# Performance work log

Measured on AMD Instinct MI355X. Metric: run time of the kernel, lower is better.

Reference implementation:

```python
import jax, jax.numpy as jnp
import numpy as np

B, S, E, H, MAXLEN = 2, 2048, 1024, 16, 2048


def _level_indices(seq_len: int, base: int = 2) -> np.ndarray:
    """Vectorized version of get_level_index_weak over the full (target, source) grid.
    indices[t, s] = min(level, 2) for s < t, else 0. Runs in O(log S) passes."""
    tt = np.broadcast_to(np.arange(seq_len)[:, None], (seq_len, seq_len)).astype(np.int64).copy()
    ss = np.broadcast_to(np.arange(seq_len)[None, :], (seq_len, seq_len)).astype(np.int64).copy()
    res = np.zeros((seq_len, seq_len), np.int64)
    done = ~(ss < tt)  # only source < target positions get a level; rest stay 0
    while not done.all():
        l = np.floor(np.log2(np.maximum(tt, 1).astype(np.float64))).astype(np.int64)
        v = (np.int64(1) << l)
        hit = (~done) & (ss < v)
        res[hit] = l[hit] + 1
        done |= hit
        step = ~done
        tt[step] -= v[step]
        ss[step] -= v[step]
    return np.minimum(res, 2).astype(np.int32)


def setup_inputs() -> dict:
    key = jax.random.key(0)
    ks = jax.random.split(key, 10)
    sc = 0.02
    return {
        "x": jax.random.normal(ks[0], (B, S, E), dtype=jnp.float32),
        "attention_mask": jax.random.randint(ks[1], (B, S), 0, 2, dtype=jnp.int32),
        "level_indices": jnp.asarray(_level_indices(S, 2)),
        "Wq": jax.random.normal(ks[2], (E, E), dtype=jnp.float32) * sc,
        "bq": jnp.zeros((E,), jnp.float32),
        "Wk": jax.random.normal(ks[3], (E, E), dtype=jnp.float32) * sc,
        "bk": jnp.zeros((E,), jnp.float32),
        "Wv": jax.random.normal(ks[4], (E, E), dtype=jnp.float32) * sc,
        "bv": jnp.zeros((E,), jnp.float32),
        "hier": jax.random.normal(ks[5], (MAXLEN, H, 3), dtype=jnp.float32),
        "Wo": jax.random.normal(ks[6], (E, E), dtype=jnp.float32) * sc,
        "bo": jnp.zeros((E,), jnp.float32),
    }


def reference(x, attention_mask, level_indices, Wq, bq, Wk, bk, Wv, bv, hier, Wo, bo):
    b, s, e = x.shape
    h = hier.shape[1]
    dh = e // h
    # q/k are computed by the original module but never used; kept for fidelity (zero grads).
    q = x @ Wq.T + bq
    k = x @ Wk.T + bk
    v = (x @ Wv.T + bv).reshape(b, s, h, dh).transpose(0, 2, 1, 3)  # [B,H,S,Dh]
    lev = level_indices[:s, :s]  # [S,S] int, values in {0,1,2}
    # Faithful torch.gather semantics: weights[b,h,i,j] = hier[b, h, lev[i,j]]
    w3 = hier[:b]                      # [B,H,3]
    weights = w3[:, :, lev]            # [B,H,S,S]
    decay = jnp.power(jnp.float32(0.5), lev.astype(x.dtype))  # [S,S]
    weights = weights * decay
    weights = weights / (jnp.sum(weights, axis=-1, keepdims=True) + 1e-8)
    weights = jnp.where(attention_mask[:, None, None, :] == 0, jnp.float32(0.0), weights)
    out = jnp.einsum('bhij,bhjd->bhid', weights, v)  # [B,H,S,Dh]
    out = out.transpose(0, 2, 1, 3).reshape(b, s, e)
    return out @ Wo.T + bo
```

## Files before the change

### kernel.cpp

```cpp
#include <hip/hip_runtime.h>
#include <cstdint>
#include <cstddef>

constexpr int Sn = 2048;
constexpr int En = 1024;
constexpr int Bn = 2;
constexpr int Hn = 16;
constexpr int CHUNK = 32;
constexpr int NCH = Sn / CHUNK;
constexpr int Mtot = Bn * Sn;
constexpr int GCH = Mtot / CHUNK;

typedef __bf16 bf16x8 __attribute__((ext_vector_type(8)));
typedef float  f32x4  __attribute__((ext_vector_type(4)));

__device__ __forceinline__ unsigned short f2bf(float f) {
    union { float f; uint32_t u; } v; v.f = f;
    const uint32_t u = v.u;
    return (unsigned short)((u + 0x7fffu + ((u >> 16) & 1u)) >> 16);
}
__device__ __forceinline__ float bf2f(unsigned short s) {
    union { uint32_t u; float f; } v; v.u = (uint32_t)s << 16; return v.f;
}

constexpr int XN = Bn * Sn * En;
constexpr int WN = En * En;

__global__ __launch_bounds__(256)
void cast2(const float* __restrict__ x, const float* __restrict__ Wv,
           unsigned short* __restrict__ xb, unsigned short* __restrict__ Wvb)
{
    const int i = (blockIdx.x * 256 + threadIdx.x) * 4;
    const float* src; unsigned short* dst; int off;
    if (i < XN) { src = x;  dst = xb;  off = i; }
    else        { src = Wv; dst = Wvb; off = i - XN; }
    const float4 v = *(const float4*)(src + off);
    ushort4 o;
    o.x = f2bf(v.x); o.y = f2bf(v.y); o.z = f2bf(v.z); o.w = f2bf(v.w);
    *(ushort4*)(dst + off) = o;
}

#define LOAD6(k0, r0, r1, r2, r3, r4, r5)            \
    r0 = *(const uint4*)(gA0 + (k0));                \
    r1 = *(const uint4*)(gA0 + (k0) + 32);           \
    r2 = *(const uint4*)(gA1 + (k0));                \
    r3 = *(const uint4*)(gA1 + (k0) + 32);           \
    r4 = *(const uint4*)(gB0 + (k0));                \
    r5 = *(const uint4*)(gB0 + (k0) + 32);

#define STORE6B(B, r0, r1, r2, r3, r4, r5)                       \
    *(uint4*)&As[B][(rg0 * 2 + 0) * 512 + lane * 8] = r0;        \
    *(uint4*)&As[B][(rg0 * 2 + 1) * 512 + lane * 8] = r1;        \
    *(uint4*)&As[B][(rg1 * 2 + 0) * 512 + lane * 8] = r2;        \
    *(uint4*)&As[B][(rg1 * 2 + 1) * 512 + lane * 8] = r3;        \
    *(uint4*)&Bs[B][(wv  * 2 + 0) * 512 + lane * 8] = r4;        \
    *(uint4*)&Bs[B][(wv  * 2 + 1) * 512 + lane * 8] = r5;

#define COMPUTEB(B)                                                                            \
    {                                                                                          \
        bf16x8 af[4][2], bfr[2][2];                                                            \
        _Pragma("unroll")                                                                      \
        for (int i = 0; i < 4; ++i)                                                            \
            _Pragma("unroll")                                                                  \
            for (int kh = 0; kh < 2; ++kh)                                                     \
                af[i][kh] = *(const bf16x8*)&As[B][((wr * 4 + i) * 2 + kh) * 512 + lane * 8];   \
        _Pragma("unroll")                                                                      \
        for (int j = 0; j < 2; ++j)                                                            \
            _Pragma("unroll")                                                                  \
            for (int kh = 0; kh < 2; ++kh)                                                     \
                bfr[j][kh] = *(const bf16x8*)&Bs[B][((wc * 2 + j) * 2 + kh) * 512 + lane * 8]; \
        _Pragma("unroll")                                                                      \
        for (int kh = 0; kh < 2; ++kh)                                                         \
            _Pragma("unroll")                                                                  \
            for (int i = 0; i < 4; ++i)                                                        \
                _Pragma("unroll")                                                              \
                for (int j = 0; j < 2; ++j)                                                    \
                    acc[i][j] = __builtin_amdgcn_mfma_f32_16x16x32_bf16(af[i][kh], bfr[j][kh], \
                                                                        acc[i][j], 0, 0, 0);   \
    }

template<bool APPLY_MASK, bool OUT_BF16, bool FUSE_CSUM>
__global__ __launch_bounds__(256)
void gemm_pipe(const unsigned short* __restrict__ A, const unsigned short* __restrict__ Bw,
               const float* __restrict__ bias, const int* __restrict__ mask,
               void* __restrict__ Cv, float* __restrict__ csum)
{
    __shared__ __align__(16) unsigned short As[2][128 * 64];
    __shared__ __align__(16) unsigned short Bs[2][64 * 64];

    const int tid  = threadIdx.x;
    const int lane = tid & 63;
    const int wv   = tid >> 6;
    const int wr   = wv >> 1;
    const int wc   = wv & 1;
    const int id   = blockIdx.y * 16 + blockIdx.x;
    const int xcd  = id & 7;
    const int slot = id >> 3;
    const int by   = xcd * 4 + (slot >> 4);
    const int bx   = slot & 15;
    const int bm   = by * 128;
    const int bn   = bx * 64;
    const int m16  = lane & 15;
    const int kq   = lane >> 4;

    f32x4 acc[4][2] = {};

    const int rg0 = 2 * wv, rg1 = 2 * wv + 1;
    const unsigned short* gA0 = A  + (size_t)(bm + 16 * rg0 + m16) * En + kq * 8;
    const unsigned short* gA1 = A  + (size_t)(bm + 16 * rg1 + m16) * En + kq * 8;
    const unsigned short* gB0 = Bw + (size_t)(bn + 16 * wv  + m16) * En + kq * 8;

    uint4 p0, p1, p2, p3, p4, p5;
    uint4 q0, q1, q2, q3, q4, q5;

    LOAD6(0,  p0, p1, p2, p3, p4, p5);
    STORE6B(0, p0, p1, p2, p3, p4, p5);
    LOAD6(64, q0, q1, q2, q3, q4, q5);
    __syncthreads();

#pragma unroll 1
    for (int it = 0; it < 7; ++it) {
        const int kb = it * 128;
        LOAD6(kb + 128, p0, p1, p2, p3, p4, p5);
        COMPUTEB(0);
        STORE6B(1, q0, q1, q2, q3, q4, q5);
        __syncthreads();
        LOAD6(kb + 192, q0, q1, q2, q3, q4, q5);
        COMPUTEB(1);
        STORE6B(0, p0, p1, p2, p3, p4, p5);
        __syncthreads();
    }
    COMPUTEB(0);
    STORE6B(1, q0, q1, q2, q3, q4, q5);
    __syncthreads();
    COMPUTEB(1);

    float colsum[2][2] = {{0.0f, 0.0f}, {0.0f, 0.0f}};
#pragma unroll
    for (int i = 0; i < 4; ++i) {
        const int r0_ = bm + wr * 64 + i * 16 + kq * 4;
#pragma unroll
        for (int j = 0; j < 2; ++j) {
            const int c0 = bn + wc * 32 + j * 16 + m16;
            const float bcol = bias[c0];
#pragma unroll
            for (int r = 0; r < 4; ++r) {
                const int row = r0_ + r;
                float val = acc[i][j][r] + bcol;
                if (APPLY_MASK) val = (mask[row] == 0) ? 0.0f : val;
                if (FUSE_CSUM) colsum[i >> 1][j] += val;
                if (OUT_BF16)
                    ((unsigned short*)Cv)[(size_t)row * En + c0] = f2bf(val);
                else
                    ((float*)Cv)[(size_t)row * En + c0] = val;
            }
        }
    }

    if (FUSE_CSUM) {
        const int gc0 = 4 * by + 2 * wr;
#pragma unroll
        for (int g = 0; g < 2; ++g)
#pragma unroll
            for (int j = 0; j < 2; ++j) {
                float s = colsum[g][j];
                s += __shfl_xor(s, 16, 64);
                s += __shfl_xor(s, 32, 64);
                if (kq == 0)
                    csum[(size_t)(gc0 + g) * En + bn + wc * 32 + j * 16 + m16] = s;
            }
    }
}

__global__ __launch_bounds__(256)
void combine(const unsigned short* __restrict__ vm, const float* __restrict__ csum,
             const float* __restrict__ hier, const float* __restrict__ Wo,
             unsigned short* __restrict__ Wob, unsigned short* __restrict__ opre)
{
    __shared__ __align__(16) unsigned short tile[CHUNK * 256];

    const int tid = threadIdx.x;
    const int ec0 = blockIdx.x * 256;
    const int c   = blockIdx.y;
    const int b   = blockIdx.z;

    {
        const int lane16 = tid & 31;
        const int rbase  = tid >> 5;
        const size_t g0 = ((size_t)b * Sn + c * CHUNK) * En + ec0 + lane16 * 8;
#pragma unroll
        for (int r4 = 0; r4 < 4; ++r4) {
            const int row = r4 * 8 + rbase;
            *(uint4*)&tile[row * 256 + lane16 * 8] =
                *(const uint4*)(vm + g0 + (size_t)row * En);
        }
    }

    {
        const int fid = (blockIdx.z * 64 + blockIdx.y) * 4 + blockIdx.x;
        const int base = fid * 2048 + tid * 4;
#pragma unroll
        for (int half = 0; half < 2; ++half) {
            const int off = base + half * 1024;
            const float4 v = *(const float4*)(Wo + off);
            ushort4 o;
            o.x = f2bf(v.x); o.y = f2bf(v.y); o.z = f2bf(v.z); o.w = f2bf(v.w);
            *(ushort4*)(Wob + off) = o;
        }
    }

    const int e = ec0 + tid;
    const int h = e >> 6;
    const float w0 = hier[((size_t)b * Hn + h) * 3 + 0];
    const float w1 = hier[((size_t)b * Hn + h) * 3 + 1] * 0.5f;
    const float w2 = hier[((size_t)b * Hn + h) * 3 + 2] * 0.25f;

    float run = 0.0f, T = 0.0f;
    {
        const float* cp = csum + (size_t)b * NCH * En + e;
#pragma unroll 16
        for (int c2 = 0; c2 < NCH; ++c2) {
            const float v = cp[(size_t)c2 * En];
            T += v;
            run += (c2 < c) ? v : 0.0f;
        }
    }

    __syncthreads();

    float prev = 0.0f;
    const size_t base = ((size_t)b * Sn + c * CHUNK) * En + e;

#pragma unroll
    for (int t = 0; t < CHUNK; ++t) {
        const int i = c * CHUNK + t;
        const float cur = bf2f(tile[t * 256 + tid]);
        float num, Z;
        if (i & 1) {
            num = w2 * (run - prev) + w1 * prev + w0 * (T - run);
            Z = (float)(i - 1) * w2 + w1 + (float)(Sn - i) * w0 + 1e-8f;
        } else {
            num = w2 * run + w0 * (T - run);
            Z = (float)i * w2 + (float)(Sn - i) * w0 + 1e-8f;
        }
        opre[base + (size_t)t * En] = f2bf(num / Z);
        run += cur;
        prev = cur;
    }
}

extern "C" void kernel_launch(void* const* d_in, const int* in_sizes, int n_in,
                              void* d_out, int out_size, void* d_ws, size_t ws_size,
                              hipStream_t stream)
{
    const float* x    = (const float*)d_in[0];
    const int*   mask = (const int*)d_in[1];
    const float* Wv   = (const float*)d_in[7];
    const float* bv   = (const float*)d_in[8];
    const float* hier = (const float*)d_in[9];
    const float* Wo   = (const float*)d_in[10];
    const float* bo   = (const float*)d_in[11];
    float* out = (float*)d_out;

    char* ws = (char*)d_ws;
    unsigned short* xb    = (unsigned short*)ws;  ws += (size_t)Mtot * En * 2;
    unsigned short* Wvb   = (unsigned short*)ws;  ws += (size_t)En * En * 2;
    unsigned short* Wob   = (unsigned short*)ws;  ws += (size_t)En * En * 2;
    unsigned short* vmb   = (unsigned short*)ws;  ws += (size_t)Mtot * En * 2;
    float*          csum  = (float*)ws;           ws += (size_t)GCH * En * 4;
    unsigned short* opreb = (unsigned short*)ws;  ws += (size_t)Mtot * En * 2;

    dim3 threads(256);

    cast2<<<dim3((XN + WN) / 1024), threads, 0, stream>>>(x, Wv, xb, Wvb);

    dim3 gemm_grid(16, 32);

    gemm_pipe<true, true, true><<<gemm_grid, threads, 0, stream>>>(xb, Wvb, bv, mask, vmb, csum);
    combine<<<dim3(En / 256, NCH, Bn), threads, 0, stream>>>(vmb, csum, hier, Wo, Wob, opreb);
    gemm_pipe<false, false, false><<<gemm_grid, threads, 0, stream>>>(opreb, Wob, bo, nullptr, out, nullptr);
}
```

Baseline: 163.1 us.

## Replace LDS double-buffered GEMM with direct global-to-register fragment loads

Removes the shared-memory staging and double-buffer pipeline in both GEMMs; each wave now loads its MFMA operand fragments directly from global memory. This removes LDS stores, LDS reads and block barriers, and frees LDS for occupancy. In exchange, A and B tiles are no longer shared across waves in a block, which raises global/L2 traffic and exposes load latency with less explicit prefetching.

New measurement: 211.1 us. 1.29x slower.

```diff
diff --git a/kernel.cpp b/kernel.cpp
--- a/kernel.cpp
+++ b/kernel.cpp
@@ -40,54 +40,12 @@
     *(ushort4*)(dst + off) = o;
 }
 
-#define LOAD6(k0, r0, r1, r2, r3, r4, r5)            \
-    r0 = *(const uint4*)(gA0 + (k0));                \
-    r1 = *(const uint4*)(gA0 + (k0) + 32);           \
-    r2 = *(const uint4*)(gA1 + (k0));                \
-    r3 = *(const uint4*)(gA1 + (k0) + 32);           \
-    r4 = *(const uint4*)(gB0 + (k0));                \
-    r5 = *(const uint4*)(gB0 + (k0) + 32);
-
-#define STORE6B(B, r0, r1, r2, r3, r4, r5)                       \
-    *(uint4*)&As[B][(rg0 * 2 + 0) * 512 + lane * 8] = r0;        \
-    *(uint4*)&As[B][(rg0 * 2 + 1) * 512 + lane * 8] = r1;        \
-    *(uint4*)&As[B][(rg1 * 2 + 0) * 512 + lane * 8] = r2;        \
-    *(uint4*)&As[B][(rg1 * 2 + 1) * 512 + lane * 8] = r3;        \
-    *(uint4*)&Bs[B][(wv  * 2 + 0) * 512 + lane * 8] = r4;        \
-    *(uint4*)&Bs[B][(wv  * 2 + 1) * 512 + lane * 8] = r5;
-
-#define COMPUTEB(B)                                                                            \
-    {                                                                                          \
-        bf16x8 af[4][2], bfr[2][2];                                                            \
-        _Pragma("unroll")                                                                      \
-        for (int i = 0; i < 4; ++i)                                                            \
-            _Pragma("unroll")                                                                  \
-            for (int kh = 0; kh < 2; ++kh)                                                     \
-                af[i][kh] = *(const bf16x8*)&As[B][((wr * 4 + i) * 2 + kh) * 512 + lane * 8];   \
-        _Pragma("unroll")                                                                      \
-        for (int j = 0; j < 2; ++j)                                                            \
-            _Pragma("unroll")                                                                  \
-            for (int kh = 0; kh < 2; ++kh)                                                     \
-                bfr[j][kh] = *(const bf16x8*)&Bs[B][((wc * 2 + j) * 2 + kh) * 512 + lane * 8]; \
-        _Pragma("unroll")                                                                      \
-        for (int kh = 0; kh < 2; ++kh)                                                         \
-            _Pragma("unroll")                                                                  \
-            for (int i = 0; i < 4; ++i)                                                        \
-                _Pragma("unroll")                                                              \
-                for (int j = 0; j < 2; ++j)                                                    \
-                    acc[i][j] = __builtin_amdgcn_mfma_f32_16x16x32_bf16(af[i][kh], bfr[j][kh], \
-                                                                        acc[i][j], 0, 0, 0);   \
-    }
-
 template<bool APPLY_MASK, bool OUT_BF16, bool FUSE_CSUM>
 __global__ __launch_bounds__(256)
-void gemm_pipe(const unsigned short* __restrict__ A, const unsigned short* __restrict__ Bw,
-               const float* __restrict__ bias, const int* __restrict__ mask,
-               void* __restrict__ Cv, float* __restrict__ csum)
-{
-    __shared__ __align__(16) unsigned short As[2][128 * 64];
-    __shared__ __align__(16) unsigned short Bs[2][64 * 64];
-
+void gemm_direct(const unsigned short* __restrict__ A, const unsigned short* __restrict__ Bw,
+                 const float* __restrict__ bias, const int* __restrict__ mask,
+                 void* __restrict__ Cv, float* __restrict__ csum)
+{
     const int tid  = threadIdx.x;
     const int lane = tid & 63;
     const int wv   = tid >> 6;
@@ -105,35 +63,38 @@
 
     f32x4 acc[4][2] = {};
 
-    const int rg0 = 2 * wv, rg1 = 2 * wv + 1;
-    const unsigned short* gA0 = A  + (size_t)(bm + 16 * rg0 + m16) * En + kq * 8;
-    const unsigned short* gA1 = A  + (size_t)(bm + 16 * rg1 + m16) * En + kq * 8;
-    const unsigned short* gB0 = Bw + (size_t)(bn + 16 * wv  + m16) * En + kq * 8;
-
-    uint4 p0, p1, p2, p3, p4, p5;
-    uint4 q0, q1, q2, q3, q4, q5;
-
-    LOAD6(0,  p0, p1, p2, p3, p4, p5);
-    STORE6B(0, p0, p1, p2, p3, p4, p5);
-    LOAD6(64, q0, q1, q2, q3, q4, q5);
-    __syncthreads();
-
-#pragma unroll 1
-    for (int it = 0; it < 7; ++it) {
-        const int kb = it * 128;
-        LOAD6(kb + 128, p0, p1, p2, p3, p4, p5);
-        COMPUTEB(0);
-        STORE6B(1, q0, q1, q2, q3, q4, q5);
-        __syncthreads();
-        LOAD6(kb + 192, q0, q1, q2, q3, q4, q5);
-        COMPUTEB(1);
-        STORE6B(0, p0, p1, p2, p3, p4, p5);
-        __syncthreads();
-    }
-    COMPUTEB(0);
-    STORE6B(1, q0, q1, q2, q3, q4, q5);
-    __syncthreads();
-    COMPUTEB(1);
+    const unsigned short* pA[4];
+    const unsigned short* pB[2];
+#pragma unroll
+    for (int i = 0; i < 4; ++i)
+        pA[i] = A + (size_t)(bm + 16 * (wr * 4 + i) + m16) * En + kq * 8;
+#pragma unroll
+    for (int j = 0; j < 2; ++j)
+        pB[j] = Bw + (size_t)(bn + 16 * (wc * 2 + j) + m16) * En + kq * 8;
+
+#pragma unroll 2
+    for (int it = 0; it < 16; ++it) {
+        const int kb = it * 64;
+        bf16x8 af[4][2], bfr[2][2];
+#pragma unroll
+        for (int i = 0; i < 4; ++i)
+#pragma unroll
+            for (int kh = 0; kh < 2; ++kh)
+                af[i][kh] = *(const bf16x8*)(pA[i] + kb + kh * 32);
+#pragma unroll
+        for (int j = 0; j < 2; ++j)
+#pragma unroll
+            for (int kh = 0; kh < 2; ++kh)
+                bfr[j][kh] = *(const bf16x8*)(pB[j] + kb + kh * 32);
+#pragma unroll
+        for (int kh = 0; kh < 2; ++kh)
+#pragma unroll
+            for (int i = 0; i < 4; ++i)
+#pragma unroll
+                for (int j = 0; j < 2; ++j)
+                    acc[i][j] = __builtin_amdgcn_mfma_f32_16x16x32_bf16(af[i][kh], bfr[j][kh],
+                                                                        acc[i][j], 0, 0, 0);
+    }
 
     float colsum[2][2] = {{0.0f, 0.0f}, {0.0f, 0.0f}};
 #pragma unroll
@@ -276,7 +237,7 @@
 
     dim3 gemm_grid(16, 32);
 
-    gemm_pipe<true, true, true><<<gemm_grid, threads, 0, stream>>>(xb, Wvb, bv, mask, vmb, csum);
+    gemm_direct<true, true, true><<<gemm_grid, threads, 0, stream>>>(xb, Wvb, bv, mask, vmb, csum);
     combine<<<dim3(En / 256, NCH, Bn), threads, 0, stream>>>(vmb, csum, hier, Wo, Wob, opreb);
-    gemm_pipe<false, false, false><<<gemm_grid, threads, 0, stream>>>(opreb, Wob, bo, nullptr, out, nullptr);
-}
+    gemm_direct<false, false, false><<<gemm_grid, threads, 0, stream>>>(opreb, Wob, bo, nullptr, out, nullptr);
+}
```

## Split-K the V projection GEMM with 128x128 tiles and merge partials in combine

Applied to the files above, without the earlier changes.

The first GEMM moves from 128x64 tiles to 128x128 tiles with a split-K of two along z, so it still launches 512 blocks and now requests two blocks per CU. Each K-half writes its own bf16 partial output and column sums, and the combine kernel adds the two partials while loading its tile and scanning the sums. The goal is more data reuse per block while keeping enough parallelism. The cost is a second partial buffer, so combine reads twice the V traffic. Rounding each partial to bf16 before summing also adds precision error.

After: 162.4 us. Within noise of the previous version (-0.4%).

```diff
diff --git a/kernel.cpp b/kernel.cpp
--- a/kernel.cpp
+++ b/kernel.cpp
@@ -40,6 +40,144 @@
     *(ushort4*)(dst + off) = o;
 }
 
+
+#define LOAD8(k0, a0, a1, a2, a3, b0, b1, b2, b3)    \
+    a0 = *(const uint4*)(gA0 + (k0));                \
+    a1 = *(const uint4*)(gA0 + (k0) + 32);           \
+    a2 = *(const uint4*)(gA1 + (k0));                \
+    a3 = *(const uint4*)(gA1 + (k0) + 32);           \
+    b0 = *(const uint4*)(gB0 + (k0));                \
+    b1 = *(const uint4*)(gB0 + (k0) + 32);           \
+    b2 = *(const uint4*)(gB1 + (k0));                \
+    b3 = *(const uint4*)(gB1 + (k0) + 32);
+
+#define STORE8B(B, a0, a1, a2, a3, b0, b1, b2, b3)               \
+    *(uint4*)&As[B][(rg0 * 2 + 0) * 512 + lane * 8] = a0;        \
+    *(uint4*)&As[B][(rg0 * 2 + 1) * 512 + lane * 8] = a1;        \
+    *(uint4*)&As[B][(rg1 * 2 + 0) * 512 + lane * 8] = a2;        \
+    *(uint4*)&As[B][(rg1 * 2 + 1) * 512 + lane * 8] = a3;        \
+    *(uint4*)&Bs[B][(rg0 * 2 + 0) * 512 + lane * 8] = b0;        \
+    *(uint4*)&Bs[B][(rg0 * 2 + 1) * 512 + lane * 8] = b1;        \
+    *(uint4*)&Bs[B][(rg1 * 2 + 0) * 512 + lane * 8] = b2;        \
+    *(uint4*)&Bs[B][(rg1 * 2 + 1) * 512 + lane * 8] = b3;
+
+#define COMPUTE44(B)                                                                           \
+    {                                                                                          \
+        bf16x8 af[4][2], bfr[4][2];                                                            \
+        _Pragma("unroll")                                                                      \
+        for (int i = 0; i < 4; ++i)                                                            \
+            _Pragma("unroll")                                                                  \
+            for (int kh = 0; kh < 2; ++kh)                                                     \
+                af[i][kh] = *(const bf16x8*)&As[B][((wr * 4 + i) * 2 + kh) * 512 + lane * 8];   \
+        _Pragma("unroll")                                                                      \
+        for (int j = 0; j < 4; ++j)                                                            \
+            _Pragma("unroll")                                                                  \
+            for (int kh = 0; kh < 2; ++kh)                                                     \
+                bfr[j][kh] = *(const bf16x8*)&Bs[B][((wc * 4 + j) * 2 + kh) * 512 + lane * 8]; \
+        _Pragma("unroll")                                                                      \
+        for (int kh = 0; kh < 2; ++kh)                                                         \
+            _Pragma("unroll")                                                                  \
+            for (int i = 0; i < 4; ++i)                                                        \
+                _Pragma("unroll")                                                              \
+                for (int j = 0; j < 4; ++j)                                                    \
+                    acc[i][j] = __builtin_amdgcn_mfma_f32_16x16x32_bf16(af[i][kh], bfr[j][kh], \
+                                                                        acc[i][j], 0, 0, 0);   \
+    }
+
+__global__ __launch_bounds__(256, 2)
+void gemm1_sk128(const unsigned short* __restrict__ A, const unsigned short* __restrict__ Bw,
+                 const float* __restrict__ bias, const int* __restrict__ mask,
+                 unsigned short* __restrict__ vm0, unsigned short* __restrict__ vm1,
+                 float* __restrict__ csum0, float* __restrict__ csum1)
+{
+    __shared__ __align__(16) unsigned short As[2][128 * 64];
+    __shared__ __align__(16) unsigned short Bs[2][128 * 64];
+
+    const int tid  = threadIdx.x;
+    const int lane = tid & 63;
+    const int wv   = tid >> 6;
+    const int wr   = wv >> 1;
+    const int wc   = wv & 1;
+    const int id   = blockIdx.y * 8 + blockIdx.x;
+    const int xcd  = id & 7;
+    const int slot = id >> 3;
+    const int by   = xcd * 4 + (slot >> 3);
+    const int bx   = slot & 7;
+    const int bm   = by * 128;
+    const int bn   = bx * 128;
+    const int m16  = lane & 15;
+    const int kq   = lane >> 4;
+    const int ks   = blockIdx.z;
+
+    f32x4 acc[4][4] = {};
+
+    const int rg0 = 2 * wv, rg1 = 2 * wv + 1;
+    const size_t koff = (size_t)ks * 512;
+    const unsigned short* gA0 = A  + (size_t)(bm + 16 * rg0 + m16) * En + koff + kq * 8;
+    const unsigned short* gA1 = A  + (size_t)(bm + 16 * rg1 + m16) * En + koff + kq * 8;
+    const unsigned short* gB0 = Bw + (size_t)(bn + 16 * rg0 + m16) * En + koff + kq * 8;
+    const unsigned short* gB1 = Bw + (size_t)(bn + 16 * rg1 + m16) * En + koff + kq * 8;
+
+    uint4 p0, p1, p2, p3, p4, p5, p6, p7;
+    uint4 q0, q1, q2, q3, q4, q5, q6, q7;
+
+    LOAD8(0,  p0, p1, p2, p3, p4, p5, p6, p7);
+    STORE8B(0, p0, p1, p2, p3, p4, p5, p6, p7);
+    LOAD8(64, q0, q1, q2, q3, q4, q5, q6, q7);
+    __syncthreads();
+
+#pragma unroll 1
+    for (int it = 0; it < 3; ++it) {
+        const int kb = it * 128;
+        LOAD8(kb + 128, p0, p1, p2, p3, p4, p5, p6, p7);
+        COMPUTE44(0);
+        STORE8B(1, q0, q1, q2, q3, q4, q5, q6, q7);
+        __syncthreads();
+        LOAD8(kb + 192, q0, q1, q2, q3, q4, q5, q6, q7);
+        COMPUTE44(1);
+        STORE8B(0, p0, p1, p2, p3, p4, p5, p6, p7);
+        __syncthreads();
+    }
+    COMPUTE44(0);
+    STORE8B(1, q0, q1, q2, q3, q4, q5, q6, q7);
+    __syncthreads();
+    COMPUTE44(1);
+
+    unsigned short* vmk = ks ? vm1 : vm0;
+    float*          csk = ks ? csum1 : csum0;
+    float colsum[2][4] = {};
+#pragma unroll
+    for (int i = 0; i < 4; ++i) {
+        const int r0_ = bm + wr * 64 + i * 16 + kq * 4;
+#pragma unroll
+        for (int j = 0; j < 4; ++j) {
+            const int c0 = bn + wc * 64 + j * 16 + m16;
+            const float bcol = (ks == 0) ? bias[c0] : 0.0f;
+#pragma unroll
+            for (int r = 0; r < 4; ++r) {
+                const int row = r0_ + r;
+                float val = acc[i][j][r] + bcol;
+                val = (mask[row] == 0) ? 0.0f : val;
+                colsum[i >> 1][j] += val;
+                vmk[(size_t)row * En + c0] = f2bf(val);
+            }
+        }
+    }
+    {
+        const int gc0 = 4 * by + 2 * wr;
+#pragma unroll
+        for (int g = 0; g < 2; ++g)
+#pragma unroll
+            for (int j = 0; j < 4; ++j) {
+                float s = colsum[g][j];
+                s += __shfl_xor(s, 16, 64);
+                s += __shfl_xor(s, 32, 64);
+                if (kq == 0)
+                    csk[(size_t)(gc0 + g) * En + bn + wc * 64 + j * 16 + m16] = s;
+            }
+    }
+}
+
 #define LOAD6(k0, r0, r1, r2, r3, r4, r5)            \
     r0 = *(const uint4*)(gA0 + (k0));                \
     r1 = *(const uint4*)(gA0 + (k0) + 32);           \
@@ -79,11 +217,9 @@
                                                                         acc[i][j], 0, 0, 0);   \
     }
 
-template<bool APPLY_MASK, bool OUT_BF16, bool FUSE_CSUM>
 __global__ __launch_bounds__(256)
-void gemm_pipe(const unsigned short* __restrict__ A, const unsigned short* __restrict__ Bw,
-               const float* __restrict__ bias, const int* __restrict__ mask,
-               void* __restrict__ Cv, float* __restrict__ csum)
+void gemm2_pipe(const unsigned short* __restrict__ A, const unsigned short* __restrict__ Bw,
+                const float* __restrict__ bias, float* __restrict__ Cv)
 {
     __shared__ __align__(16) unsigned short As[2][128 * 64];
     __shared__ __align__(16) unsigned short Bs[2][64 * 64];
@@ -135,7 +271,6 @@
     __syncthreads();
     COMPUTEB(1);
 
-    float colsum[2][2] = {{0.0f, 0.0f}, {0.0f, 0.0f}};
 #pragma unroll
     for (int i = 0; i < 4; ++i) {
         const int r0_ = bm + wr * 64 + i * 16 + kq * 4;
@@ -144,40 +279,20 @@
             const int c0 = bn + wc * 32 + j * 16 + m16;
             const float bcol = bias[c0];
 #pragma unroll
-            for (int r = 0; r < 4; ++r) {
-                const int row = r0_ + r;
-                float val = acc[i][j][r] + bcol;
-                if (APPLY_MASK) val = (mask[row] == 0) ? 0.0f : val;
-                if (FUSE_CSUM) colsum[i >> 1][j] += val;
-                if (OUT_BF16)
-                    ((unsigned short*)Cv)[(size_t)row * En + c0] = f2bf(val);
-                else
-                    ((float*)Cv)[(size_t)row * En + c0] = val;
-            }
-        }
-    }
-
-    if (FUSE_CSUM) {
-        const int gc0 = 4 * by + 2 * wr;
-#pragma unroll
-        for (int g = 0; g < 2; ++g)
-#pragma unroll
-            for (int j = 0; j < 2; ++j) {
-                float s = colsum[g][j];
-                s += __shfl_xor(s, 16, 64);
-                s += __shfl_xor(s, 32, 64);
-                if (kq == 0)
-                    csum[(size_t)(gc0 + g) * En + bn + wc * 32 + j * 16 + m16] = s;
-            }
+            for (int r = 0; r < 4; ++r)
+                Cv[(size_t)(r0_ + r) * En + c0] = acc[i][j][r] + bcol;
+        }
     }
 }
 
 __global__ __launch_bounds__(256)
-void combine(const unsigned short* __restrict__ vm, const float* __restrict__ csum,
+void combine(const unsigned short* __restrict__ vm0, const unsigned short* __restrict__ vm1,
+             const float* __restrict__ csum0, const float* __restrict__ csum1,
              const float* __restrict__ hier, const float* __restrict__ Wo,
              unsigned short* __restrict__ Wob, unsigned short* __restrict__ opre)
 {
-    __shared__ __align__(16) unsigned short tile[CHUNK * 256];
+    __shared__ __align__(16) unsigned short tile0[CHUNK * 256];
+    __shared__ __align__(16) unsigned short tile1[CHUNK * 256];
 
     const int tid = threadIdx.x;
     const int ec0 = blockIdx.x * 256;
@@ -191,8 +306,10 @@
 #pragma unroll
         for (int r4 = 0; r4 < 4; ++r4) {
             const int row = r4 * 8 + rbase;
-            *(uint4*)&tile[row * 256 + lane16 * 8] =
-                *(const uint4*)(vm + g0 + (size_t)row * En);
+            *(uint4*)&tile0[row * 256 + lane16 * 8] =
+                *(const uint4*)(vm0 + g0 + (size_t)row * En);
+            *(uint4*)&tile1[row * 256 + lane16 * 8] =
+                *(const uint4*)(vm1 + g0 + (size_t)row * En);
         }
     }
 
@@ -217,10 +334,11 @@
 
     float run = 0.0f, T = 0.0f;
     {
-        const float* cp = csum + (size_t)b * NCH * En + e;
+        const float* cp0 = csum0 + (size_t)b * NCH * En + e;
+        const float* cp1 = csum1 + (size_t)b * NCH * En + e;
 #pragma unroll 16
         for (int c2 = 0; c2 < NCH; ++c2) {
-            const float v = cp[(size_t)c2 * En];
+            const float v = cp0[(size_t)c2 * En] + cp1[(size_t)c2 * En];
             T += v;
             run += (c2 < c) ? v : 0.0f;
         }
@@ -234,7 +352,7 @@
 #pragma unroll
     for (int t = 0; t < CHUNK; ++t) {
         const int i = c * CHUNK + t;
-        const float cur = bf2f(tile[t * 256 + tid]);
+        const float cur = bf2f(tile0[t * 256 + tid]) + bf2f(tile1[t * 256 + tid]);
         float num, Z;
         if (i & 1) {
             num = w2 * (run - prev) + w1 * prev + w0 * (T - run);
@@ -266,17 +384,19 @@
     unsigned short* xb    = (unsigned short*)ws;  ws += (size_t)Mtot * En * 2;
     unsigned short* Wvb   = (unsigned short*)ws;  ws += (size_t)En * En * 2;
     unsigned short* Wob   = (unsigned short*)ws;  ws += (size_t)En * En * 2;
-    unsigned short* vmb   = (unsigned short*)ws;  ws += (size_t)Mtot * En * 2;
-    float*          csum  = (float*)ws;           ws += (size_t)GCH * En * 4;
+    unsigned short* vmb0  = (unsigned short*)ws;  ws += (size_t)Mtot * En * 2;
+    unsigned short* vmb1  = (unsigned short*)ws;  ws += (size_t)Mtot * En * 2;
+    float*          csum0 = (float*)ws;           ws += (size_t)GCH * En * 4;
+    float*          csum1 = (float*)ws;           ws += (size_t)GCH * En * 4;
     unsigned short* opreb = (unsigned short*)ws;  ws += (size_t)Mtot * En * 2;
 
     dim3 threads(256);
 
     cast2<<<dim3((XN + WN) / 1024), threads, 0, stream>>>(x, Wv, xb, Wvb);
 
-    dim3 gemm_grid(16, 32);
-
-    gemm_pipe<true, true, true><<<gemm_grid, threads, 0, stream>>>(xb, Wvb, bv, mask, vmb, csum);
-    combine<<<dim3(En / 256, NCH, Bn), threads, 0, stream>>>(vmb, csum, hier, Wo, Wob, opreb);
-    gemm_pipe<false, false, false><<<gemm_grid, threads, 0, stream>>>(opreb, Wob, bo, nullptr, out, nullptr);
-}
+    gemm1_sk128<<<dim3(8, 32, 2), threads, 0, stream>>>(xb, Wvb, bv, mask,
+                                                        vmb0, vmb1, csum0, csum1);
+    combine<<<dim3(En / 256, NCH, Bn), threads, 0, stream>>>(vmb0, vmb1, csum0, csum1,
+                                                             hier, Wo, Wob, opreb);
+    gemm2_pipe<<<dim3(16, 32), threads, 0, stream>>>(opreb, Wob, bo, out);
+}
```
